# Optimization experiments

Hardware: AMD Instinct MI355X
Metric: run time of the kernel (lower is better)

The kernel has to match this reference:

```python
import jax, jax.numpy as jnp
import numpy as np

N = 20000
E = 320000
G = 512
BN_EPS = 1e-5


def setup_inputs() -> dict:
    key = jax.random.key(0)
    ks = jax.random.split(key, 32)
    def nrm(i, shape, s=0.05):
        return jax.random.normal(ks[i], shape, dtype=jnp.float32) * s
    inp = {}
    inp["x"] = jax.random.normal(ks[0], (N, 64), dtype=jnp.float32)
    inp["edge_index"] = jax.random.randint(ks[1], (2, E), 0, N)
    inp["edge_attr"] = jax.random.normal(ks[2], (E, 32), dtype=jnp.float32)
    inp["batch"] = jnp.sort(jax.random.randint(ks[3], (N,), 0, G))
    # GINEConv 1: edge lin 32->64, nn Linear 64->256
    inp["we1"] = nrm(4, (64, 32));  inp["be1"] = jnp.zeros((64,), jnp.float32)
    inp["wn1"] = nrm(5, (256, 64)); inp["bnb1"] = jnp.zeros((256,), jnp.float32)
    # GINEConv 2: edge lin 32->256, nn Linear 256->256
    inp["we2"] = nrm(6, (256, 32)); inp["be2"] = jnp.zeros((256,), jnp.float32)
    inp["wn2"] = nrm(7, (256, 256)); inp["bnb2"] = jnp.zeros((256,), jnp.float32)
    # GINEConv 3
    inp["we3"] = nrm(8, (256, 32)); inp["be3"] = jnp.zeros((256,), jnp.float32)
    inp["wn3"] = nrm(9, (256, 256)); inp["bnb3"] = jnp.zeros((256,), jnp.float32)
    # BatchNorm params (eval mode: running stats)
    for li, ki in ((1, 10), (2, 11), (3, 12)):
        inp[f"g{li}"] = jnp.ones((256,), jnp.float32)
        inp[f"b{li}"] = jnp.zeros((256,), jnp.float32)
        inp[f"rm{li}"] = nrm(ki, (256,), 0.01)
        inp[f"rv{li}"] = jnp.ones((256,), jnp.float32)
    # Head: Linear 256->128, Linear 128->1
    inp["w4"] = nrm(13, (128, 256)); inp["b4"] = jnp.zeros((128,), jnp.float32)
    inp["w5"] = nrm(14, (1, 128));   inp["b5"] = jnp.zeros((1,), jnp.float32)
    return inp


def _gine(x, src, dst, e, we, be, wn, bnb):
    # message = ReLU(x_j + Lin(edge_attr)); aggr = scatter-sum over dst; out = nn(x + aggr)
    m = jax.nn.relu(x[src] + e @ we.T + be)            # [E, d_in]
    aggr = jax.ops.segment_sum(m, dst, num_segments=x.shape[0])
    return (x + aggr) @ wn.T + bnb                      # [N, hidden]


def _bn_relu(h, g, b, rm, rv):
    return jax.nn.relu((h - rm) * jax.lax.rsqrt(rv + BN_EPS) * g + b)


def reference(x, edge_index, edge_attr, batch,
              we1, be1, wn1, bnb1, we2, be2, wn2, bnb2, we3, be3, wn3, bnb3,
              g1, b1, rm1, rv1, g2, b2, rm2, rv2, g3, b3, rm3, rv3,
              w4, b4, w5, b5):
    src, dst = edge_index[0], edge_index[1]
    h = _bn_relu(_gine(x, src, dst, edge_attr, we1, be1, wn1, bnb1), g1, b1, rm1, rv1)
    h = _bn_relu(_gine(h, src, dst, edge_attr, we2, be2, wn2, bnb2), g2, b2, rm2, rv2)
    h = _bn_relu(_gine(h, src, dst, edge_attr, we3, be3, wn3, bnb3), g3, b3, rm3, rv3)
    # global mean pool over graphs
    sums = jax.ops.segment_sum(h, batch, num_segments=G)                 # [G, 256]
    cnt = jax.ops.segment_sum(jnp.ones((h.shape[0],), h.dtype), batch, num_segments=G)
    pooled = sums / jnp.maximum(cnt, 1.0)[:, None]
    # dropout is identity in eval mode
    z = jax.nn.relu(pooled @ w4.T + b4)
    return jax.nn.sigmoid(z @ w5.T + b5)                                 # [G, 1]
```

## Files before the change

### kernel.cpp

```cpp
#include <hip/hip_runtime.h>
#include <hip/hip_bf16.h>
#include <math.h>


typedef __attribute__((ext_vector_type(8))) short short8v;
typedef __attribute__((ext_vector_type(4))) float f32x4;
typedef __attribute__((ext_vector_type(4))) unsigned short us4;
typedef __attribute__((ext_vector_type(8))) unsigned short us8;

static __device__ __forceinline__ float bf2f(unsigned short u) {
    union { unsigned int u32; float f; } c; c.u32 = ((unsigned int)u) << 16; return c.f;
}
static __device__ __forceinline__ unsigned short f2bf(float f) {
    union { float f; unsigned int u; } c; c.f = f;
    unsigned int lsb = (c.u >> 16) & 1u;
    c.u += 0x7fffu + lsb;
    return (unsigned short)(c.u >> 16);
}

__global__ void k_zero_i(int* __restrict__ p, int n) {
    int i = blockIdx.x * blockDim.x + threadIdx.x;
    int st = gridDim.x * blockDim.x;
    for (; i < n; i += st) p[i] = 0;
}

__global__ void k_hist2(const int* __restrict__ dst, int E,
                        const int* __restrict__ batch, int N,
                        int* __restrict__ ideg, int* __restrict__ gcnt) {
    int b = blockIdx.x;
    if (b < 512) {
        int i = b * 256 + threadIdx.x, st = 512 * 256;
        for (; i < E; i += st) atomicAdd(&ideg[dst[i]], 1);
    } else {
        int i = (b - 512) * 256 + threadIdx.x, st = 128 * 256;
        for (; i < N; i += st) atomicAdd(&gcnt[batch[i]], 1);
    }
}

__global__ __launch_bounds__(256) void k_scan_part(const int* __restrict__ in,
                                                   int* __restrict__ part, int n) {
    __shared__ int wtot[4];
    const int tid = threadIdx.x, lane = tid & 63, wv = tid >> 6;
    int i = blockIdx.x * 256 + tid;
    int s = (i < n) ? in[i] : 0;
#pragma unroll
    for (int off = 1; off < 64; off <<= 1) s += __shfl_xor(s, off);
    if (lane == 0) wtot[wv] = s;
    __syncthreads();
    if (tid == 0) part[blockIdx.x] = wtot[0] + wtot[1] + wtot[2] + wtot[3];
}

static __device__ void scan_block(const int* __restrict__ in, int* __restrict__ out,
                                  int n, int* wsum) {
    const int tid = threadIdx.x;
    const int lane = tid & 63, wv = tid >> 6;
    const int C = (n + 1023) >> 10;
    const int base = tid * C;
    int s = 0;
    for (int k = 0; k < C; ++k) {
        int i = base + k;
        if (i < n) s += in[i];
    }
    int incl = s;
#pragma unroll
    for (int off = 1; off < 64; off <<= 1) {
        int t = __shfl_up(incl, off);
        if (lane >= off) incl += t;
    }
    if (lane == 63) wsum[wv] = incl;
    __syncthreads();
    int woff = 0;
    for (int i2 = 0; i2 < wv; ++i2) woff += wsum[i2];
    int run = woff + incl - s;
    for (int k = 0; k < C; ++k) {
        int i = base + k;
        if (i < n) {
            out[i] = run;
            run += in[i];
        }
    }
    if (tid == 1023) out[n] = run;
    __syncthreads();
}

__global__ __launch_bounds__(1024) void k_scan_mid(
    const int* __restrict__ part, int* __restrict__ part_s, int npart,
    const int* __restrict__ gcnt, int* __restrict__ gptr, int G,
    int* __restrict__ rowptr, int N) {
    __shared__ int wsum[16];
    scan_block(part, part_s, npart, wsum);
    if (threadIdx.x == 0) rowptr[N] = part_s[npart];
    scan_block(gcnt, gptr, G, wsum);
}

__global__ __launch_bounds__(256) void k_scan_out(const int* __restrict__ in,
                                                  const int* __restrict__ part_s,
                                                  int* __restrict__ rowptr,
                                                  int* __restrict__ cursor, int n) {
    __shared__ int wtot[4];
    const int tid = threadIdx.x, lane = tid & 63, wv = tid >> 6;
    int i = blockIdx.x * 256 + tid;
    int v = (i < n) ? in[i] : 0;
    int s = v;
#pragma unroll
    for (int off = 1; off < 64; off <<= 1) {
        int t = __shfl_up(s, off);
        if (lane >= off) s += t;
    }
    if (lane == 63) wtot[wv] = s;
    __syncthreads();
    int woff = 0;
    for (int k = 0; k < wv; ++k) woff += wtot[k];
    int excl = part_s[blockIdx.x] + woff + s - v;
    if (i < n) { rowptr[i] = excl; cursor[i] = excl; }
}

__global__ void k_scatter(const int* __restrict__ ei, const float* __restrict__ ea,
                          int E, int Epad, int* __restrict__ cursor,
                          int* __restrict__ esrc_s, int* __restrict__ dst_s,
                          unsigned short* __restrict__ ea_s) {
    int i = blockIdx.x * blockDim.x + threadIdx.x;
    int st = gridDim.x * blockDim.x;
    for (int k = i; k < E; k += st) {
        int d = ei[E + k];
        int pos = atomicAdd(&cursor[d], 1);
        esrc_s[pos] = ei[k];
        dst_s[pos] = d;
        const float4* sp = (const float4*)(ea + (size_t)k * 32);
        unsigned short* dp = ea_s + (size_t)pos * 32;
#pragma unroll
        for (int h = 0; h < 4; ++h) {
            float4 a = sp[2 * h], b = sp[2 * h + 1];
            us8 o;
            o[0] = f2bf(a.x); o[1] = f2bf(a.y); o[2] = f2bf(a.z); o[3] = f2bf(a.w);
            o[4] = f2bf(b.x); o[5] = f2bf(b.y); o[6] = f2bf(b.z); o[7] = f2bf(b.w);
            *(us8*)(dp + h * 8) = o;
        }
    }
    if (i < Epad + 64 - E) {
        dst_s[E + i] = -1;
        if (i < Epad - E) {
            esrc_s[E + i] = 0;
            us4 z = {0, 0, 0, 0};
            us4* p = (us4*)(ea_s + (size_t)(E + i) * 32);
#pragma unroll
            for (int q = 0; q < 8; ++q) p[q] = z;
        }
    }
}

__global__ void k_wxprep(const float* __restrict__ we1, const float* __restrict__ we2,
                         const float* __restrict__ we3, const float* __restrict__ wn1,
                         const float* __restrict__ wn2, const float* __restrict__ wn3,
                         const float* __restrict__ w4, const float* __restrict__ x,
                         unsigned short* __restrict__ webf1, unsigned short* __restrict__ webf2,
                         unsigned short* __restrict__ webf3, unsigned short* __restrict__ wnbf1,
                         unsigned short* __restrict__ wnbf2, unsigned short* __restrict__ wnbf3,
                         float* __restrict__ w4t, unsigned short* __restrict__ x_bf,
                         float* __restrict__ aggrA, int n16) {
    int idx = blockIdx.x * blockDim.x + threadIdx.x;
    if (idx >= 49664) {
        int i = idx - 49664;
        if (i < n16) {
            int n = i >> 4, j = i & 15;
            float4 t = *(const float4*)(x + (size_t)n * 64 + j * 4);
            ((float4*)aggrA)[i] = t;
            us4 o;
            o.x = f2bf(x[(size_t)n * 64 + j]);
            o.y = f2bf(x[(size_t)n * 64 + 16 + j]);
            o.z = f2bf(x[(size_t)n * 64 + 32 + j]);
            o.w = f2bf(x[(size_t)n * 64 + 48 + j]);
            *(us4*)(x_bf + (size_t)n * 64 + j * 4) = o;
        }
        return;
    }
    const float* s; unsigned short* d; int rel;
    if (idx < 512)        { s = we1; d = webf1; rel = idx; }
    else if (idx < 2560)  { s = we2; d = webf2; rel = idx - 512; }
    else if (idx < 4608)  { s = we3; d = webf3; rel = idx - 2560; }
    else if (idx < 8704)  { s = wn1; d = wnbf1; rel = idx - 4608; }
    else if (idx < 25088) { s = wn2; d = wnbf2; rel = idx - 8704; }
    else if (idx < 41472) { s = wn3; d = wnbf3; rel = idx - 25088; }
    else {
        int rel2 = idx - 41472;
        int k = rel2 >> 5;
        int j0 = (rel2 & 31) * 4;
        int ck = (k & 0xC0) | (((k & 3) * 16) + ((k & 63) >> 2));
        float4 o;
        o.x = w4[(j0 + 0) * 256 + ck]; o.y = w4[(j0 + 1) * 256 + ck];
        o.z = w4[(j0 + 2) * 256 + ck]; o.w = w4[(j0 + 3) * 256 + ck];
        *(float4*)(w4t + k * 128 + j0) = o;
        return;
    }
    float4 t = ((const float4*)s)[rel];
    us4 o; o.x = f2bf(t.x); o.y = f2bf(t.y); o.z = f2bf(t.z); o.w = f2bf(t.w);
    ((us4*)d)[rel] = o;
}

template<int D>
__global__ __launch_bounds__(256) void k_edge_mfma(
    const unsigned short* __restrict__ hbf,
    const unsigned short* __restrict__ ea_s,
    const int* __restrict__ esrc_s,
    const int* __restrict__ dst_s,
    const unsigned short* __restrict__ webf,
    const float* __restrict__ be,
    float* __restrict__ aggr,
    int E)
{
    const int tid = threadIdx.x;
    const int lane = tid & 63;
    const int w = tid >> 6;
    const int l15 = lane & 15;
    const int lhi = lane >> 4;

    const int wavetile = (D == 256) ? (int)blockIdx.x : ((int)blockIdx.x * 4 + w);
    const int colbase  = (D == 256) ? (w * 64) : 0;
    const int e0 = wavetile * 64;
    if (e0 >= E) return;

    const int dstreg = dst_s[e0 + lane];

    int4 src4[4];
#pragma unroll
    for (int q = 0; q < 4; ++q)
        src4[q] = *(const int4*)(esrc_s + e0 + q * 16 + lhi * 4);

    short8v afr[4];
#pragma unroll
    for (int q = 0; q < 4; ++q)
        afr[q] = *(const short8v*)(ea_s + (size_t)(e0 + q * 16 + l15) * 32 + lhi * 8);

    short8v bfr[4]; float bias[4];
#pragma unroll
    for (int t = 0; t < 4; ++t) {
        int c = colbase + t * 16 + l15;
        bfr[t] = *(const short8v*)(webf + (size_t)c * 32 + lhi * 8);
        bias[t] = be[c];
    }

    us4 hv[4][4];
#pragma unroll
    for (int q = 0; q < 4; ++q) {
        const int sr[4] = {src4[q].x, src4[q].y, src4[q].z, src4[q].w};
#pragma unroll
        for (int i = 0; i < 4; ++i)
            hv[q][i] = *(const us4*)(hbf + (size_t)sr[i] * D + colbase + l15 * 4);
    }

    f32x4 acc[4][4];
#pragma unroll
    for (int q = 0; q < 4; ++q)
#pragma unroll
        for (int t = 0; t < 4; ++t) {
            f32x4 ci; ci[0] = bias[t]; ci[1] = bias[t]; ci[2] = bias[t]; ci[3] = bias[t];
            acc[q][t] = __builtin_amdgcn_mfma_f32_16x16x32_bf16(afr[q], bfr[t], ci, 0, 0, 0);
        }

#pragma unroll
    for (int q = 0; q < 4; ++q)
#pragma unroll
        for (int i = 0; i < 4; ++i) {
            us4 h4 = hv[q][i];
#pragma unroll
            for (int t = 0; t < 4; ++t)
                acc[q][t][i] = fmaxf(acc[q][t][i] + bf2f(h4[t]), 0.0f);
        }

    float carry[4] = {0.0f, 0.0f, 0.0f, 0.0f};
#pragma unroll
    for (int q = 0; q < 4; ++q)
#pragma unroll
        for (int t = 0; t < 4; ++t) {
            acc[q][t][1] += acc[q][t][0];
            acc[q][t][2] += acc[q][t][1];
            acc[q][t][3] += acc[q][t][2];
            float g = acc[q][t][3];
            float g1 = __shfl_up(g, 16);
            if (lhi >= 1) g += g1;
            float g2 = __shfl_up(g, 32);
            if (lhi >= 2) g += g2;
            float tqv = __shfl(g, 48 + l15);
            float excl = g - acc[q][t][3] + carry[t];
            acc[q][t][0] += excl; acc[q][t][1] += excl;
            acc[q][t][2] += excl; acc[q][t][3] += excl;
            carry[t] += tqv;
        }

    int dnext = __shfl_down(dstreg, 1);
    bool endf = (lane == 63) || (dstreg != dnext);
    unsigned long long mask = __ballot(endf);

    float prevP[4] = {0.0f, 0.0f, 0.0f, 0.0f};
    while (mask) {
        int r = __builtin_amdgcn_readfirstlane((int)__builtin_ctzll(mask));
        mask &= mask - 1;
        int dseg = __shfl(dstreg, r);
        int sl = ((r >> 2) & 3) * 16 + l15;
        float curP[4];
        switch (((r >> 4) << 2) | (r & 3)) {
#define CASE_QI(Q, I) \
            case ((Q) * 4 + (I)): \
                curP[0] = __shfl(acc[Q][0][I], sl); curP[1] = __shfl(acc[Q][1][I], sl); \
                curP[2] = __shfl(acc[Q][2][I], sl); curP[3] = __shfl(acc[Q][3][I], sl); \
                break;
            CASE_QI(0,0) CASE_QI(0,1) CASE_QI(0,2) CASE_QI(0,3)
            CASE_QI(1,0) CASE_QI(1,1) CASE_QI(1,2) CASE_QI(1,3)
            CASE_QI(2,0) CASE_QI(2,1) CASE_QI(2,2) CASE_QI(2,3)
            CASE_QI(3,0) CASE_QI(3,1) CASE_QI(3,2) CASE_QI(3,3)
#undef CASE_QI
        }
        if (dseg >= 0 && lhi == 0) {
            float* base = aggr + (size_t)dseg * D + colbase + l15;
#pragma unroll
            for (int t = 0; t < 4; ++t)
                atomicAdd(base + t * 16, curP[t] - prevP[t]);
        }
#pragma unroll
        for (int t = 0; t < 4; ++t) prevP[t] = curP[t];
    }
}

template<int K, bool AW>
__global__ __launch_bounds__(256) void k_node_mfma(
    const float* __restrict__ A, const unsigned short* __restrict__ wnbf,
    const float* __restrict__ bnb, const float* __restrict__ g,
    const float* __restrict__ b, const float* __restrict__ rm,
    const float* __restrict__ rv, unsigned short* __restrict__ out,
    float* __restrict__ aggr_out, int N)
{
    const int tid = threadIdx.x;
    const int lane = tid & 63;
    const int w = tid >> 6;
    const int l15 = lane & 15;
    const int lhi = lane >> 4;
    const int row0 = blockIdx.x * 64;
    const int ncol0 = w * 64;

    f32x4 scale[4], shift[4];
    f32x4 acc[4][4];
#pragma unroll
    for (int q = 0; q < 4; ++q) {
        int n0 = ncol0 + q * 16 + lhi * 4;
        float4 gg = *(const float4*)(g + n0);
        float4 rvv = *(const float4*)(rv + n0);
        float4 bb = *(const float4*)(b + n0);
        float4 rmm = *(const float4*)(rm + n0);
        float4 bn = *(const float4*)(bnb + n0);
        f32x4 sc, sh, ci;
        sc[0] = gg.x * rsqrtf(rvv.x + 1e-5f);
        sc[1] = gg.y * rsqrtf(rvv.y + 1e-5f);
        sc[2] = gg.z * rsqrtf(rvv.z + 1e-5f);
        sc[3] = gg.w * rsqrtf(rvv.w + 1e-5f);
        sh[0] = bb.x - rmm.x * sc[0];
        sh[1] = bb.y - rmm.y * sc[1];
        sh[2] = bb.z - rmm.z * sc[2];
        sh[3] = bb.w - rmm.w * sc[3];
        ci[0] = bn.x; ci[1] = bn.y; ci[2] = bn.z; ci[3] = bn.w;
        scale[q] = sc; shift[q] = sh;
#pragma unroll
        for (int r = 0; r < 4; ++r) acc[q][r] = ci;
    }

    for (int k0 = 0; k0 < K; k0 += 32) {
        short8v wfr[4];
#pragma unroll
        for (int q = 0; q < 4; ++q)
            wfr[q] = *(const short8v*)(wnbf + (size_t)(ncol0 + q * 16 + l15) * K + k0 + lhi * 8);
        short8v afr[4];
#pragma unroll
        for (int r = 0; r < 4; ++r) {
            const float* ap = A + (size_t)(row0 + r * 16 + l15) * K + k0 + lhi * 8;
            float4 a0 = ((const float4*)ap)[0];
            float4 a1 = ((const float4*)ap)[1];
            short8v t;
            t[0] = (short)f2bf(a0.x); t[1] = (short)f2bf(a0.y);
            t[2] = (short)f2bf(a0.z); t[3] = (short)f2bf(a0.w);
            t[4] = (short)f2bf(a1.x); t[5] = (short)f2bf(a1.y);
            t[6] = (short)f2bf(a1.z); t[7] = (short)f2bf(a1.w);
            afr[r] = t;
        }
#pragma unroll
        for (int q = 0; q < 4; ++q)
#pragma unroll
            for (int r = 0; r < 4; ++r)
                acc[q][r] = __builtin_amdgcn_mfma_f32_16x16x32_bf16(wfr[q], afr[r], acc[q][r], 0, 0, 0);
    }

#pragma unroll
    for (int r = 0; r < 4; ++r) {
        int m = row0 + r * 16 + l15;
        if (m < N) {
            f32x4 o4[4];
#pragma unroll
            for (int q = 0; q < 4; ++q) {
                int n0 = ncol0 + q * 16 + lhi * 4;
                f32x4 v = acc[q][r];
                f32x4 o;
#pragma unroll
                for (int i = 0; i < 4; ++i)
                    o[i] = fmaxf(v[i] * scale[q][i] + shift[q][i], 0.0f);
                o4[q] = o;
                if (AW) *(f32x4*)(aggr_out + (size_t)m * 256 + n0) = o;
            }
            us8 lo, hi;
#pragma unroll
            for (int q = 0; q < 4; ++q)
#pragma unroll
                for (int i = 0; i < 4; ++i) {
                    int p = i * 4 + q;
                    unsigned short v = f2bf(o4[q][i]);
                    if (p < 8) lo[p] = v; else hi[p - 8] = v;
                }
            *(us8*)(out + (size_t)m * 256 + ncol0 + lhi * 16) = lo;
            *(us8*)(out + (size_t)m * 256 + ncol0 + lhi * 16 + 8) = hi;
        }
    }
}

__global__ __launch_bounds__(256) void k_pool_head(
    const unsigned short* __restrict__ h, const int* __restrict__ gptr,
    const float* __restrict__ w4t, const float* __restrict__ b4,
    const float* __restrict__ w5, const float* __restrict__ b5,
    float* __restrict__ out)
{
    __shared__ float pl[256];
    __shared__ float zs[128];
    const int g = blockIdx.x;
    const int tid = threadIdx.x;
    int beg = gptr[g], end = gptr[g + 1];
    float acc = 0.0f;
    for (int r = beg; r < end; ++r) acc += bf2f(h[(size_t)r * 256 + tid]);
    float cnt = (float)(end - beg);
    pl[tid] = acc / fmaxf(cnt, 1.0f);
    __syncthreads();
    if (tid < 128) {
        float a = b4[tid];
        for (int k = 0; k < 256; ++k) a += pl[k] * w4t[k * 128 + tid];
        zs[tid] = fmaxf(a, 0.0f);
    }
    __syncthreads();
    if (tid < 64) {
        float v = zs[tid] * w5[tid] + zs[tid + 64] * w5[tid + 64];
#pragma unroll
        for (int off = 32; off > 0; off >>= 1) v += __shfl_down(v, off);
        if (tid == 0) out[g] = 1.0f / (1.0f + expf(-(v + b5[0])));
    }
}

extern "C" void kernel_launch(void* const* d_in, const int* in_sizes, int n_in,
                              void* d_out, int out_size, void* d_ws, size_t ws_size,
                              hipStream_t stream)
{
    const float* x    = (const float*)d_in[0];
    const int*   ei   = (const int*)d_in[1];
    const float* ea   = (const float*)d_in[2];
    const int*   batch= (const int*)d_in[3];
    const float* we1  = (const float*)d_in[4];
    const float* be1  = (const float*)d_in[5];
    const float* wn1  = (const float*)d_in[6];
    const float* bnb1 = (const float*)d_in[7];
    const float* we2  = (const float*)d_in[8];
    const float* be2  = (const float*)d_in[9];
    const float* wn2  = (const float*)d_in[10];
    const float* bnb2 = (const float*)d_in[11];
    const float* we3  = (const float*)d_in[12];
    const float* be3  = (const float*)d_in[13];
    const float* wn3  = (const float*)d_in[14];
    const float* bnb3 = (const float*)d_in[15];
    const float* g1 = (const float*)d_in[16];
    const float* b1 = (const float*)d_in[17];
    const float* rm1= (const float*)d_in[18];
    const float* rv1= (const float*)d_in[19];
    const float* g2 = (const float*)d_in[20];
    const float* b2 = (const float*)d_in[21];
    const float* rm2= (const float*)d_in[22];
    const float* rv2= (const float*)d_in[23];
    const float* g3 = (const float*)d_in[24];
    const float* b3 = (const float*)d_in[25];
    const float* rm3= (const float*)d_in[26];
    const float* rv3= (const float*)d_in[27];
    const float* w4 = (const float*)d_in[28];
    const float* b4 = (const float*)d_in[29];
    const float* w5 = (const float*)d_in[30];
    const float* b5 = (const float*)d_in[31];

    const int N = in_sizes[0] / 64;
    const int E = in_sizes[1] / 2;
    const int G = out_size;
    const int Epad = (E + 63) & ~63;
    const int npart = (N + 255) / 256;

    float* ws    = (float*)d_ws;
    float* aggrA = ws;
    float* aggrB = aggrA + (size_t)N * 256;
    float* w4t   = aggrB + (size_t)N * 256;
    unsigned short* ea_s  = (unsigned short*)(w4t + 256 * 128);
    unsigned short* x_bf  = ea_s + (size_t)Epad * 32;
    unsigned short* h_bf  = x_bf + (size_t)N * 64;
    unsigned short* webf1 = h_bf + (size_t)N * 256;
    unsigned short* webf2 = webf1 + 64 * 32;
    unsigned short* webf3 = webf2 + 256 * 32;
    unsigned short* wnbf1 = webf3 + 256 * 32;
    unsigned short* wnbf2 = wnbf1 + 256 * 64;
    unsigned short* wnbf3 = wnbf2 + 256 * 256;
    int* iws    = (int*)(wnbf3 + 256 * 256);
    int* ideg   = iws;
    int* gcnt   = ideg + N;
    int* rowptr = gcnt + G;
    int* gptr   = rowptr + N + 16;
    int* cursor = gptr + G + 16;
    int* esrc_s = cursor + N;
    int* dst_s  = esrc_s + Epad;
    int* part   = dst_s + Epad + 64;
    int* part_s = part + npart;

    const int nblk64  = (N + 63) / 64;
    const int eblk256 = (E + 63) / 64;
    const int eblk64  = (E + 255) / 256;

    k_zero_i<<<64, 256, 0, stream>>>(ideg, N + G);
    k_hist2<<<640, 256, 0, stream>>>(ei + E, E, batch, N, ideg, gcnt);
    k_scan_part<<<npart, 256, 0, stream>>>(ideg, part, N);
    k_scan_mid<<<1, 1024, 0, stream>>>(part, part_s, npart, gcnt, gptr, G, rowptr, N);
    k_scan_out<<<npart, 256, 0, stream>>>(ideg, part_s, rowptr, cursor, N);
    k_scatter<<<512, 256, 0, stream>>>(ei, ea, E, Epad, cursor, esrc_s, dst_s, ea_s);
    k_wxprep<<<(49664 + 320000 + 255) / 256, 256, 0, stream>>>(
        we1, we2, we3, wn1, wn2, wn3, w4, x,
        webf1, webf2, webf3, wnbf1, wnbf2, wnbf3, w4t, x_bf, aggrA, N * 16);

    k_edge_mfma<64><<<eblk64, 256, 0, stream>>>(
        x_bf, ea_s, esrc_s, dst_s, webf1, be1, aggrA, E);
    k_node_mfma<64, true><<<nblk64, 256, 0, stream>>>(aggrA, wnbf1, bnb1, g1, b1, rm1, rv1,
                                                      h_bf, aggrB, N);

    k_edge_mfma<256><<<eblk256, 256, 0, stream>>>(
        h_bf, ea_s, esrc_s, dst_s, webf2, be2, aggrB, E);
    k_node_mfma<256, true><<<nblk64, 256, 0, stream>>>(aggrB, wnbf2, bnb2, g2, b2, rm2, rv2,
                                                       h_bf, aggrA, N);

    k_edge_mfma<256><<<eblk256, 256, 0, stream>>>(
        h_bf, ea_s, esrc_s, dst_s, webf3, be3, aggrA, E);
    k_node_mfma<256, false><<<nblk64, 256, 0, stream>>>(aggrA, wnbf3, bnb3, g3, b3, rm3, rv3,
                                                        h_bf, (float*)nullptr, N);

    k_pool_head<<<G, 256, 0, stream>>>(h_bf, gptr, w4t, b4, w5, b5, (float*)d_out);
}
```

Before: 261.8 us.

## Fuse prep kernels, eliminate mid scan, process two edge tiles per wave

```diff
diff --git a/kernel.cpp b/kernel.cpp
--- a/kernel.cpp
+++ b/kernel.cpp
@@ -24,17 +24,71 @@
     for (; i < n; i += st) p[i] = 0;
 }
 
-__global__ void k_hist2(const int* __restrict__ dst, int E,
-                        const int* __restrict__ batch, int N,
-                        int* __restrict__ ideg, int* __restrict__ gcnt) {
+__global__ void k_pre1(const int* __restrict__ dst, int E,
+                       const int* __restrict__ batch, int N,
+                       int* __restrict__ ideg, int* __restrict__ gcnt,
+                       const float* __restrict__ we1, const float* __restrict__ we2,
+                       const float* __restrict__ we3, const float* __restrict__ wn1,
+                       const float* __restrict__ wn2, const float* __restrict__ wn3,
+                       const float* __restrict__ w4, const float* __restrict__ x,
+                       unsigned short* __restrict__ webf1, unsigned short* __restrict__ webf2,
+                       unsigned short* __restrict__ webf3, unsigned short* __restrict__ wnbf1,
+                       unsigned short* __restrict__ wnbf2, unsigned short* __restrict__ wnbf3,
+                       float* __restrict__ w4p, unsigned short* __restrict__ x_bf,
+                       float* __restrict__ aggrA, int n16) {
     int b = blockIdx.x;
     if (b < 512) {
         int i = b * 256 + threadIdx.x, st = 512 * 256;
         for (; i < E; i += st) atomicAdd(&ideg[dst[i]], 1);
-    } else {
+        return;
+    }
+    if (b < 640) {
         int i = (b - 512) * 256 + threadIdx.x, st = 128 * 256;
         for (; i < N; i += st) atomicAdd(&gcnt[batch[i]], 1);
-    }
+        return;
+    }
+    int idx = (b - 640) * 256 + threadIdx.x;
+    if (idx >= 49664) {
+        int i = idx - 49664;
+        if (i < n16) {
+            int n = i >> 4, j = i & 15;
+            float4 t = *(const float4*)(x + (size_t)n * 64 + j * 4);
+            ((float4*)aggrA)[i] = t;
+            us4 o;
+            o.x = f2bf(x[(size_t)n * 64 + j]);
+            o.y = f2bf(x[(size_t)n * 64 + 16 + j]);
+            o.z = f2bf(x[(size_t)n * 64 + 32 + j]);
+            o.w = f2bf(x[(size_t)n * 64 + 48 + j]);
+            *(us4*)(x_bf + (size_t)n * 64 + j * 4) = o;
+        }
+        return;
+    }
+    const float* s; unsigned short* d; int rel;
+    if (idx < 512)        { s = we1; d = webf1; rel = idx; }
+    else if (idx < 2560)  { s = we2; d = webf2; rel = idx - 512; }
+    else if (idx < 4608)  { s = we3; d = webf3; rel = idx - 2560; }
+    else if (idx < 8704)  { s = wn1; d = wnbf1; rel = idx - 4608; }
+    else if (idx < 25088) { s = wn2; d = wnbf2; rel = idx - 8704; }
+    else if (idx < 41472) { s = wn3; d = wnbf3; rel = idx - 25088; }
+    else {
+        int rel2 = idx - 41472;
+        int j = rel2 >> 6;
+        int k0 = (rel2 & 63) * 4;
+        float4 o;
+        float vv[4];
+#pragma unroll
+        for (int i = 0; i < 4; ++i) {
+            int k = k0 + i;
+            int ck = (k & 0xC0) | (((k & 3) * 16) + ((k & 63) >> 2));
+            vv[i] = w4[j * 256 + ck];
+        }
+        o.x = vv[0]; o.y = vv[1]; o.z = vv[2]; o.w = vv[3];
+        *(float4*)(w4p + j * 256 + k0) = o;
+        return;
+    }
+    float4 t = ((const float4*)s)[rel];
+    us4 o; o.x = f2bf(t.x); o.y = f2bf(t.y); o.z = f2bf(t.z); o.w = f2bf(t.w);
+    ((us4*)d)[rel] = o;
 }
 
 __global__ __launch_bounds__(256) void k_scan_part(const int* __restrict__ in,
@@ -50,56 +104,38 @@
     if (tid == 0) part[blockIdx.x] = wtot[0] + wtot[1] + wtot[2] + wtot[3];
 }
 
-static __device__ void scan_block(const int* __restrict__ in, int* __restrict__ out,
-                                  int n, int* wsum) {
-    const int tid = threadIdx.x;
-    const int lane = tid & 63, wv = tid >> 6;
-    const int C = (n + 1023) >> 10;
-    const int base = tid * C;
-    int s = 0;
-    for (int k = 0; k < C; ++k) {
-        int i = base + k;
-        if (i < n) s += in[i];
-    }
-    int incl = s;
-#pragma unroll
-    for (int off = 1; off < 64; off <<= 1) {
-        int t = __shfl_up(incl, off);
-        if (lane >= off) incl += t;
-    }
-    if (lane == 63) wsum[wv] = incl;
-    __syncthreads();
-    int woff = 0;
-    for (int i2 = 0; i2 < wv; ++i2) woff += wsum[i2];
-    int run = woff + incl - s;
-    for (int k = 0; k < C; ++k) {
-        int i = base + k;
-        if (i < n) {
-            out[i] = run;
-            run += in[i];
-        }
-    }
-    if (tid == 1023) out[n] = run;
-    __syncthreads();
-}
-
-__global__ __launch_bounds__(1024) void k_scan_mid(
-    const int* __restrict__ part, int* __restrict__ part_s, int npart,
-    const int* __restrict__ gcnt, int* __restrict__ gptr, int G,
-    int* __restrict__ rowptr, int N) {
-    __shared__ int wsum[16];
-    scan_block(part, part_s, npart, wsum);
-    if (threadIdx.x == 0) rowptr[N] = part_s[npart];
-    scan_block(gcnt, gptr, G, wsum);
-}
-
 __global__ __launch_bounds__(256) void k_scan_out(const int* __restrict__ in,
-                                                  const int* __restrict__ part_s,
-                                                  int* __restrict__ rowptr,
-                                                  int* __restrict__ cursor, int n) {
+                                                  const int* __restrict__ part,
+                                                  int* __restrict__ cursor, int n, int npart,
+                                                  const int* __restrict__ gcnt,
+                                                  int* __restrict__ gptr, int G) {
+    const int tid = threadIdx.x, lane = tid & 63, wv = tid >> 6;
+    if ((int)blockIdx.x == npart) {
+        if (tid < 64) {
+            int run = 0;
+            for (int c = 0; c < G; c += 64) {
+                int v = gcnt[c + lane];
+                int s = v;
+#pragma unroll
+                for (int off = 1; off < 64; off <<= 1) {
+                    int t = __shfl_up(s, off);
+                    if (lane >= off) s += t;
+                }
+                gptr[c + lane] = run + s - v;
+                run += __shfl(s, 63);
+            }
+            if (lane == 0) gptr[G] = run;
+        }
+        return;
+    }
     __shared__ int wtot[4];
-    const int tid = threadIdx.x, lane = tid & 63, wv = tid >> 6;
-    int i = blockIdx.x * 256 + tid;
+    const int bid = blockIdx.x;
+    int p = 0;
+    if (lane < bid) p = part[lane];
+    if (lane + 64 < bid) p += part[lane + 64];
+#pragma unroll
+    for (int off = 1; off < 64; off <<= 1) p += __shfl_xor(p, off);
+    int i = bid * 256 + tid;
     int v = (i < n) ? in[i] : 0;
     int s = v;
 #pragma unroll
@@ -111,8 +147,7 @@
     __syncthreads();
     int woff = 0;
     for (int k = 0; k < wv; ++k) woff += wtot[k];
-    int excl = part_s[blockIdx.x] + woff + s - v;
-    if (i < n) { rowptr[i] = excl; cursor[i] = excl; }
+    if (i < n) cursor[i] = p + woff + s - v;
 }
 
 __global__ void k_scatter(const int* __restrict__ ei, const float* __restrict__ ea,
@@ -147,54 +182,6 @@
             for (int q = 0; q < 8; ++q) p[q] = z;
         }
     }
-}
-
-__global__ void k_wxprep(const float* __restrict__ we1, const float* __restrict__ we2,
-                         const float* __restrict__ we3, const float* __restrict__ wn1,
-                         const float* __restrict__ wn2, const float* __restrict__ wn3,
-                         const float* __restrict__ w4, const float* __restrict__ x,
-                         unsigned short* __restrict__ webf1, unsigned short* __restrict__ webf2,
-                         unsigned short* __restrict__ webf3, unsigned short* __restrict__ wnbf1,
-                         unsigned short* __restrict__ wnbf2, unsigned short* __restrict__ wnbf3,
-                         float* __restrict__ w4t, unsigned short* __restrict__ x_bf,
-                         float* __restrict__ aggrA, int n16) {
-    int idx = blockIdx.x * blockDim.x + threadIdx.x;
-    if (idx >= 49664) {
-        int i = idx - 49664;
-        if (i < n16) {
-            int n = i >> 4, j = i & 15;
-            float4 t = *(const float4*)(x + (size_t)n * 64 + j * 4);
-            ((float4*)aggrA)[i] = t;
-            us4 o;
-            o.x = f2bf(x[(size_t)n * 64 + j]);
-            o.y = f2bf(x[(size_t)n * 64 + 16 + j]);
-            o.z = f2bf(x[(size_t)n * 64 + 32 + j]);
-            o.w = f2bf(x[(size_t)n * 64 + 48 + j]);
-            *(us4*)(x_bf + (size_t)n * 64 + j * 4) = o;
-        }
-        return;
-    }
-    const float* s; unsigned short* d; int rel;
-    if (idx < 512)        { s = we1; d = webf1; rel = idx; }
-    else if (idx < 2560)  { s = we2; d = webf2; rel = idx - 512; }
-    else if (idx < 4608)  { s = we3; d = webf3; rel = idx - 2560; }
-    else if (idx < 8704)  { s = wn1; d = wnbf1; rel = idx - 4608; }
-    else if (idx < 25088) { s = wn2; d = wnbf2; rel = idx - 8704; }
-    else if (idx < 41472) { s = wn3; d = wnbf3; rel = idx - 25088; }
-    else {
-        int rel2 = idx - 41472;
-        int k = rel2 >> 5;
-        int j0 = (rel2 & 31) * 4;
-        int ck = (k & 0xC0) | (((k & 3) * 16) + ((k & 63) >> 2));
-        float4 o;
-        o.x = w4[(j0 + 0) * 256 + ck]; o.y = w4[(j0 + 1) * 256 + ck];
-        o.z = w4[(j0 + 2) * 256 + ck]; o.w = w4[(j0 + 3) * 256 + ck];
-        *(float4*)(w4t + k * 128 + j0) = o;
-        return;
-    }
-    float4 t = ((const float4*)s)[rel];
-    us4 o; o.x = f2bf(t.x); o.y = f2bf(t.y); o.z = f2bf(t.z); o.w = f2bf(t.w);
-    ((us4*)d)[rel] = o;
 }
 
 template<int D>
@@ -214,22 +201,9 @@
     const int l15 = lane & 15;
     const int lhi = lane >> 4;
 
-    const int wavetile = (D == 256) ? (int)blockIdx.x : ((int)blockIdx.x * 4 + w);
-    const int colbase  = (D == 256) ? (w * 64) : 0;
-    const int e0 = wavetile * 64;
-    if (e0 >= E) return;
-
-    const int dstreg = dst_s[e0 + lane];
-
-    int4 src4[4];
-#pragma unroll
-    for (int q = 0; q < 4; ++q)
-        src4[q] = *(const int4*)(esrc_s + e0 + q * 16 + lhi * 4);
-
-    short8v afr[4];
-#pragma unroll
-    for (int q = 0; q < 4; ++q)
-        afr[q] = *(const short8v*)(ea_s + (size_t)(e0 + q * 16 + l15) * 32 + lhi * 8);
+    const int tbase   = (D == 256) ? ((int)blockIdx.x * 2) : (((int)blockIdx.x * 4 + w) * 2);
+    const int colbase = (D == 256) ? (w * 64) : 0;
+    if (tbase * 64 >= E) return;
 
     short8v bfr[4]; float bias[4];
 #pragma unroll
@@ -239,85 +213,102 @@
         bias[t] = be[c];
     }
 
-    us4 hv[4][4];
-#pragma unroll
-    for (int q = 0; q < 4; ++q) {
-        const int sr[4] = {src4[q].x, src4[q].y, src4[q].z, src4[q].w};
-#pragma unroll
-        for (int i = 0; i < 4; ++i)
-            hv[q][i] = *(const us4*)(hbf + (size_t)sr[i] * D + colbase + l15 * 4);
-    }
-
-    f32x4 acc[4][4];
-#pragma unroll
-    for (int q = 0; q < 4; ++q)
-#pragma unroll
-        for (int t = 0; t < 4; ++t) {
-            f32x4 ci; ci[0] = bias[t]; ci[1] = bias[t]; ci[2] = bias[t]; ci[3] = bias[t];
-            acc[q][t] = __builtin_amdgcn_mfma_f32_16x16x32_bf16(afr[q], bfr[t], ci, 0, 0, 0);
-        }
-
-#pragma unroll
-    for (int q = 0; q < 4; ++q)
-#pragma unroll
-        for (int i = 0; i < 4; ++i) {
-            us4 h4 = hv[q][i];
-#pragma unroll
-            for (int t = 0; t < 4; ++t)
-                acc[q][t][i] = fmaxf(acc[q][t][i] + bf2f(h4[t]), 0.0f);
-        }
-
-    float carry[4] = {0.0f, 0.0f, 0.0f, 0.0f};
-#pragma unroll
-    for (int q = 0; q < 4; ++q)
-#pragma unroll
-        for (int t = 0; t < 4; ++t) {
-            acc[q][t][1] += acc[q][t][0];
-            acc[q][t][2] += acc[q][t][1];
-            acc[q][t][3] += acc[q][t][2];
-            float g = acc[q][t][3];
-            float g1 = __shfl_up(g, 16);
-            if (lhi >= 1) g += g1;
-            float g2 = __shfl_up(g, 32);
-            if (lhi >= 2) g += g2;
-            float tqv = __shfl(g, 48 + l15);
-            float excl = g - acc[q][t][3] + carry[t];
-            acc[q][t][0] += excl; acc[q][t][1] += excl;
-            acc[q][t][2] += excl; acc[q][t][3] += excl;
-            carry[t] += tqv;
-        }
-
-    int dnext = __shfl_down(dstreg, 1);
-    bool endf = (lane == 63) || (dstreg != dnext);
-    unsigned long long mask = __ballot(endf);
-
-    float prevP[4] = {0.0f, 0.0f, 0.0f, 0.0f};
-    while (mask) {
-        int r = __builtin_amdgcn_readfirstlane((int)__builtin_ctzll(mask));
-        mask &= mask - 1;
-        int dseg = __shfl(dstreg, r);
-        int sl = ((r >> 2) & 3) * 16 + l15;
-        float curP[4];
-        switch (((r >> 4) << 2) | (r & 3)) {
+    for (int tt = 0; tt < 2; ++tt) {
+        const int e0 = (tbase + tt) * 64;
+        if (e0 >= E) break;
+
+        const int dstreg = dst_s[e0 + lane];
+
+        int4 src4[4];
+#pragma unroll
+        for (int q = 0; q < 4; ++q)
+            src4[q] = *(const int4*)(esrc_s + e0 + q * 16 + lhi * 4);
+
+        short8v afr[4];
+#pragma unroll
+        for (int q = 0; q < 4; ++q)
+            afr[q] = *(const short8v*)(ea_s + (size_t)(e0 + q * 16 + l15) * 32 + lhi * 8);
+
+        us4 hv[4][4];
+#pragma unroll
+        for (int q = 0; q < 4; ++q) {
+            const int sr[4] = {src4[q].x, src4[q].y, src4[q].z, src4[q].w};
+#pragma unroll
+            for (int i = 0; i < 4; ++i)
+                hv[q][i] = *(const us4*)(hbf + (size_t)sr[i] * D + colbase + l15 * 4);
+        }
+
+        f32x4 acc[4][4];
+#pragma unroll
+        for (int q = 0; q < 4; ++q)
+#pragma unroll
+            for (int t = 0; t < 4; ++t) {
+                f32x4 ci; ci[0] = bias[t]; ci[1] = bias[t]; ci[2] = bias[t]; ci[3] = bias[t];
+                acc[q][t] = __builtin_amdgcn_mfma_f32_16x16x32_bf16(afr[q], bfr[t], ci, 0, 0, 0);
+            }
+
+#pragma unroll
+        for (int q = 0; q < 4; ++q)
+#pragma unroll
+            for (int i = 0; i < 4; ++i) {
+                us4 h4 = hv[q][i];
+#pragma unroll
+                for (int t = 0; t < 4; ++t)
+                    acc[q][t][i] = fmaxf(acc[q][t][i] + bf2f(h4[t]), 0.0f);
+            }
+
+        float carry[4] = {0.0f, 0.0f, 0.0f, 0.0f};
+#pragma unroll
+        for (int q = 0; q < 4; ++q)
+#pragma unroll
+            for (int t = 0; t < 4; ++t) {
+                acc[q][t][1] += acc[q][t][0];
+                acc[q][t][2] += acc[q][t][1];
+                acc[q][t][3] += acc[q][t][2];
+                float g = acc[q][t][3];
+                float g1 = __shfl_up(g, 16);
+                if (lhi >= 1) g += g1;
+                float g2 = __shfl_up(g, 32);
+                if (lhi >= 2) g += g2;
+                float tqv = __shfl(g, 48 + l15);
+                float excl = g - acc[q][t][3] + carry[t];
+                acc[q][t][0] += excl; acc[q][t][1] += excl;
+                acc[q][t][2] += excl; acc[q][t][3] += excl;
+                carry[t] += tqv;
+            }
+
+        int dnext = __shfl_down(dstreg, 1);
+        bool endf = (lane == 63) || (dstreg != dnext);
+        unsigned long long mask = __ballot(endf);
+
+        float prevP[4] = {0.0f, 0.0f, 0.0f, 0.0f};
+        while (mask) {
+            int r = __builtin_amdgcn_readfirstlane((int)__builtin_ctzll(mask));
+            mask &= mask - 1;
+            int dseg = __shfl(dstreg, r);
+            int sl = ((r >> 2) & 3) * 16 + l15;
+            float curP[4];
+            switch (((r >> 4) << 2) | (r & 3)) {
 #define CASE_QI(Q, I) \
-            case ((Q) * 4 + (I)): \
-                curP[0] = __shfl(acc[Q][0][I], sl); curP[1] = __shfl(acc[Q][1][I], sl); \
-                curP[2] = __shfl(acc[Q][2][I], sl); curP[3] = __shfl(acc[Q][3][I], sl); \
-                break;
-            CASE_QI(0,0) CASE_QI(0,1) CASE_QI(0,2) CASE_QI(0,3)
-            CASE_QI(1,0) CASE_QI(1,1) CASE_QI(1,2) CASE_QI(1,3)
-            CASE_QI(2,0) CASE_QI(2,1) CASE_QI(2,2) CASE_QI(2,3)
-            CASE_QI(3,0) CASE_QI(3,1) CASE_QI(3,2) CASE_QI(3,3)
+                case ((Q) * 4 + (I)): \
+                    curP[0] = __shfl(acc[Q][0][I], sl); curP[1] = __shfl(acc[Q][1][I], sl); \
+                    curP[2] = __shfl(acc[Q][2][I], sl); curP[3] = __shfl(acc[Q][3][I], sl); \
+                    break;
+                CASE_QI(0,0) CASE_QI(0,1) CASE_QI(0,2) CASE_QI(0,3)
+                CASE_QI(1,0) CASE_QI(1,1) CASE_QI(1,2) CASE_QI(1,3)
+                CASE_QI(2,0) CASE_QI(2,1) CASE_QI(2,2) CASE_QI(2,3)
+                CASE_QI(3,0) CASE_QI(3,1) CASE_QI(3,2) CASE_QI(3,3)
 #undef CASE_QI
-        }
-        if (dseg >= 0 && lhi == 0) {
-            float* base = aggr + (size_t)dseg * D + colbase + l15;
-#pragma unroll
-            for (int t = 0; t < 4; ++t)
-                atomicAdd(base + t * 16, curP[t] - prevP[t]);
-        }
-#pragma unroll
-        for (int t = 0; t < 4; ++t) prevP[t] = curP[t];
+            }
+            if (dseg >= 0 && lhi == 0) {
+                float* base = aggr + (size_t)dseg * D + colbase + l15;
+#pragma unroll
+                for (int t = 0; t < 4; ++t)
+                    atomicAdd(base + t * 16, curP[t] - prevP[t]);
+            }
+#pragma unroll
+            for (int t = 0; t < 4; ++t) prevP[t] = curP[t];
+        }
     }
 }
 
@@ -420,7 +411,7 @@
 
 __global__ __launch_bounds__(256) void k_pool_head(
     const unsigned short* __restrict__ h, const int* __restrict__ gptr,
-    const float* __restrict__ w4t, const float* __restrict__ b4,
+    const float* __restrict__ w4p, const float* __restrict__ b4,
     const float* __restrict__ w5, const float* __restrict__ b5,
     float* __restrict__ out)
 {
@@ -436,7 +427,12 @@
     __syncthreads();
     if (tid < 128) {
         float a = b4[tid];
-        for (int k = 0; k < 256; ++k) a += pl[k] * w4t[k * 128 + tid];
+        const float4* wr = (const float4*)(w4p + (size_t)tid * 256);
+        for (int k4 = 0; k4 < 64; ++k4) {
+            float4 wv = wr[k4];
+            int k = k4 * 4;
+            a += pl[k] * wv.x + pl[k + 1] * wv.y + pl[k + 2] * wv.z + pl[k + 3] * wv.w;
+        }
         zs[tid] = fmaxf(a, 0.0f);
     }
     __syncthreads();
@@ -490,12 +486,13 @@
     const int G = out_size;
     const int Epad = (E + 63) & ~63;
     const int npart = (N + 255) / 256;
+    const int n16 = N * 16;
 
     float* ws    = (float*)d_ws;
     float* aggrA = ws;
     float* aggrB = aggrA + (size_t)N * 256;
-    float* w4t   = aggrB + (size_t)N * 256;
-    unsigned short* ea_s  = (unsigned short*)(w4t + 256 * 128);
+    float* w4p   = aggrB + (size_t)N * 256;
+    unsigned short* ea_s  = (unsigned short*)(w4p + 128 * 256);
     unsigned short* x_bf  = ea_s + (size_t)Epad * 32;
     unsigned short* h_bf  = x_bf + (size_t)N * 64;
     unsigned short* webf1 = h_bf + (size_t)N * 256;
@@ -507,27 +504,25 @@
     int* iws    = (int*)(wnbf3 + 256 * 256);
     int* ideg   = iws;
     int* gcnt   = ideg + N;
-    int* rowptr = gcnt + G;
-    int* gptr   = rowptr + N + 16;
+    int* gptr   = gcnt + G;
     int* cursor = gptr + G + 16;
     int* esrc_s = cursor + N;
     int* dst_s  = esrc_s + Epad;
     int* part   = dst_s + Epad + 64;
-    int* part_s = part + npart;
 
     const int nblk64  = (N + 63) / 64;
-    const int eblk256 = (E + 63) / 64;
-    const int eblk64  = (E + 255) / 256;
+    const int ntiles  = (E + 63) / 64;
+    const int eblk256 = (ntiles + 1) / 2;
+    const int eblk64  = (ntiles + 7) / 8;
 
     k_zero_i<<<64, 256, 0, stream>>>(ideg, N + G);
-    k_hist2<<<640, 256, 0, stream>>>(ei + E, E, batch, N, ideg, gcnt);
+    k_pre1<<<640 + (49664 + n16 + 255) / 256, 256, 0, stream>>>(
+        ei + E, E, batch, N, ideg, gcnt,
+        we1, we2, we3, wn1, wn2, wn3, w4, x,
+        webf1, webf2, webf3, wnbf1, wnbf2, wnbf3, w4p, x_bf, aggrA, n16);
     k_scan_part<<<npart, 256, 0, stream>>>(ideg, part, N);
-    k_scan_mid<<<1, 1024, 0, stream>>>(part, part_s, npart, gcnt, gptr, G, rowptr, N);
-    k_scan_out<<<npart, 256, 0, stream>>>(ideg, part_s, rowptr, cursor, N);
+    k_scan_out<<<npart + 1, 256, 0, stream>>>(ideg, part, cursor, N, npart, gcnt, gptr, G);
     k_scatter<<<512, 256, 0, stream>>>(ei, ea, E, Epad, cursor, esrc_s, dst_s, ea_s);
-    k_wxprep<<<(49664 + 320000 + 255) / 256, 256, 0, stream>>>(
-        we1, we2, we3, wn1, wn2, wn3, w4, x,
-        webf1, webf2, webf3, wnbf1, wnbf2, wnbf3, w4t, x_bf, aggrA, N * 16);
 
     k_edge_mfma<64><<<eblk64, 256, 0, stream>>>(
         x_bf, ea_s, esrc_s, dst_s, webf1, be1, aggrA, E);
@@ -544,5 +539,5 @@
     k_node_mfma<256, false><<<nblk64, 256, 0, stream>>>(aggrA, wnbf3, bnb3, g3, b3, rm3, rv3,
                                                         h_bf, (float*)nullptr, N);
 
-    k_pool_head<<<G, 256, 0, stream>>>(h_bf, gptr, w4t, b4, w5, b5, (float*)d_out);
-}
+    k_pool_head<<<G, 256, 0, stream>>>(h_bf, gptr, w4p, b4, w5, b5, (float*)d_out);
+}
```

New measurement: 280.6 us. +7.2%, slower.
